# Kernel tuning notes

Hardware: AMD Instinct MI355X
Metric: run time of the kernel (lower is better)

The kernel has to match this reference:

```python
import jax, jax.numpy as jnp
import numpy as np

# --- dims (match init_kwargs) ---
B = 2048          # batch
BACK = 512        # backcast_length (in_dim of first layer)
UNITS = 512       # hidden units
FORE = 128        # forecast_length
TH = FORE         # thetas_dim (nb_harmonics=None)
NL = 4            # num_block_layers
NUM = 5           # grid intervals
K = 3             # spline order
MINP = 1          # min_period
NCOEF = NUM + K   # 8 spline coefficients per edge


def _grid(in_dim):
    # extended uniform grid over [-1,1] with K extra knots each side -> NUM+2K+1 points
    h = 2.0 / NUM
    pts = (np.arange(-K, NUM + K + 1) * h - 1.0).astype(np.float32)
    return jnp.asarray(np.tile(pts[None, :], (in_dim, 1)))


def _bspline(x, grid):
    # x: (B, in_dim), grid: (in_dim, NUM+2K+1) -> (B, in_dim, NUM+K)
    xe = x[:, :, None]
    g = grid[None]
    v = ((xe >= g[:, :, :-1]) & (xe < g[:, :, 1:])).astype(x.dtype)
    for p in range(1, K + 1):  # Cox-de Boor recursion, K is small & static
        v = (xe - g[:, :, :-(p + 1)]) / (g[:, :, p:-1] - g[:, :, :-(p + 1)]) * v[:, :, :-1] \
          + (g[:, :, p + 1:] - xe) / (g[:, :, p + 1:] - g[:, :, 1:-p]) * v[:, :, 1:]
    return v


def _kan(x, grid, coef, sb, ssp):
    # y[b,o] = sum_i sb[i,o]*silu(x[b,i]) + sum_i ssp[i,o]*sum_k B[b,i,k]*coef[i,o,k]
    # (mask == ones; scale_sp folded into coef to avoid (B,in,out) intermediate)
    bsp = _bspline(x, grid)                          # (B, in, NCOEF)
    base = jax.nn.silu(x)                            # (B, in)
    return base @ sb + jnp.einsum('bik,iok->bo', bsp, coef * ssp[:, :, None])


def _seasonal_basis():
    T = BACK + FORE
    lin = np.linspace(0.0, (T - 1) / T, T)           # linspace(centered=False)
    bl, fl = lin[:BACK], lin[BACK:]
    p1 = p2 = TH // 2                                # TH even
    f1 = np.linspace(0.0, T / MINP, p1)
    f2 = np.linspace(0.0, T / MINP, p2)
    Sb = np.concatenate([np.cos(2 * np.pi * f1[:, None] * bl),
                         np.sin(2 * np.pi * f2[:, None] * bl)]).astype(np.float32)
    Sf = np.concatenate([np.cos(2 * np.pi * f1[:, None] * fl),
                         np.sin(2 * np.pi * f2[:, None] * fl)]).astype(np.float32)
    return jnp.asarray(Sb), jnp.asarray(Sf)          # (TH, BACK), (TH, FORE)


def setup_inputs() -> dict:
    key = jax.random.key(0)
    ks = jax.random.split(key, 8)
    x = jax.random.uniform(ks[0], (B, BACK), jnp.float32, -1.0, 1.0)
    # fc KAN layers: first maps BACK->UNITS, rest UNITS->UNITS; BACK==UNITS so stack
    coef_fc = 0.1 * jax.random.normal(ks[1], (NL, UNITS, UNITS, NCOEF), jnp.float32)
    sb_fc = 0.3 * jax.random.normal(ks[2], (NL, UNITS, UNITS), jnp.float32)
    ssp_fc = 1.0 + 0.1 * jax.random.normal(ks[3], (NL, UNITS, UNITS), jnp.float32)
    # shared theta layer UNITS -> TH
    coef_th = 0.1 * jax.random.normal(ks[4], (UNITS, TH, NCOEF), jnp.float32)
    sb_th = 0.3 * jax.random.normal(ks[5], (UNITS, TH), jnp.float32)
    ssp_th = 1.0 + 0.1 * jax.random.normal(ks[6], (UNITS, TH), jnp.float32)
    return dict(x=x, coef_fc=coef_fc, sb_fc=sb_fc, ssp_fc=ssp_fc,
                coef_th=coef_th, sb_th=sb_th, ssp_th=ssp_th)


def reference(x, coef_fc, sb_fc, ssp_fc, coef_th, sb_th, ssp_th):
    grid = _grid(UNITS)  # BACK == UNITS, one grid serves all layers
    h = x
    for l in range(NL):  # static small layer loop (dropout p=0 / eval)
        h = _kan(h, grid, coef_fc[l], sb_fc[l], ssp_fc[l])
    theta = _kan(h, grid, coef_th, sb_th, ssp_th)  # theta_b_fc is theta_f_fc (shared)
    Sb, Sf = _seasonal_basis()
    backcast = theta @ Sb    # (B, BACK)
    forecast = theta @ Sf    # (B, FORE)
    return backcast, forecast
```

## Files before the change

### kernel.cpp

```cpp
#include <hip/hip_runtime.h>
#include <stdint.h>


typedef unsigned short u16;
typedef __attribute__((ext_vector_type(8))) short short8;
typedef __attribute__((ext_vector_type(4))) float f32x4;

#define NB 2048
#define KD 4608
#define NTH 128
#define NTT 640

__device__ __forceinline__ u16 f2bf(float f) {
  union { float f; uint32_t u; } c; c.f = f;
  return (u16)((c.u + 0x7FFFu + ((c.u >> 16) & 1u)) >> 16);
}

__device__ __forceinline__ void load_lds16(const void* g, void* lds) {
  __builtin_amdgcn_global_load_lds((const __attribute__((address_space(1))) void*)g,
                                   (__attribute__((address_space(3))) void*)lds, 16, 0, 0);
}

__device__ __forceinline__ void bspline8(float x, float* v8) {
  float g[12];
  #pragma unroll
  for (int j = 0; j < 12; ++j) g[j] = (float)((j - 3) * 0.4 - 1.0);
  float w[11];
  #pragma unroll
  for (int j = 0; j < 11; ++j) w[j] = (x >= g[j] && x < g[j+1]) ? 1.0f : 0.0f;
  #pragma unroll
  for (int p = 1; p <= 3; ++p) {
    #pragma unroll
    for (int j = 0; j < 11 - p; ++j) {
      const float i1 = 1.0f / (g[j+p] - g[j]);
      const float i2 = 1.0f / (g[j+p+1] - g[j+1]);
      w[j] = (x - g[j]) * i1 * w[j] + (g[j+p+1] - x) * i2 * w[j+1];
    }
  }
  #pragma unroll
  for (int j = 0; j < 8; ++j) v8[j] = w[j];
}

__device__ __forceinline__ void expand_one(float xv, u16* __restrict__ row, int i) {
  const float base = xv / (1.0f + __expf(-xv));
  float v[8];
  bspline8(xv, v);
  row[i] = f2bf(base);
  #pragma unroll
  for (int k = 0; k < 8; ++k) row[(1 + k) * 512 + i] = f2bf(v[k]);
}

__global__ __launch_bounds__(256)
void setup_kernel(const float* __restrict__ coef_fc, const float* __restrict__ sb_fc,
                  const float* __restrict__ ssp_fc,  const float* __restrict__ coef_th,
                  const float* __restrict__ sb_th,   const float* __restrict__ ssp_th,
                  u16* __restrict__ WtFc, u16* __restrict__ WtTh, float* __restrict__ S) {
  const int blk = blockIdx.x, tid = threadIdx.x;
  __shared__ u16 T[9 * 64 * 66];
  if (blk < 272) {
    const float *coef, *sb, *ssp; u16* Wt; int O, l, i0, o0;
    if (blk < 256) {
      coef = coef_fc; sb = sb_fc; ssp = ssp_fc; Wt = WtFc; O = 512;
      l = blk >> 6; i0 = ((blk >> 3) & 7) * 64; o0 = (blk & 7) * 64;
    } else {
      coef = coef_th; sb = sb_th; ssp = ssp_th; Wt = WtTh; O = 128;
      const int t = blk - 256;
      l = 0; i0 = (t >> 1) * 64; o0 = (t & 1) * 64;
    }
    #pragma unroll 4
    for (int pass = 0; pass < 16; ++pass) {
      const int o_loc = tid & 63;
      const int i_loc = pass * 4 + (tid >> 6);
      const size_t io = ((size_t)l * 512 + i0 + i_loc) * (size_t)O + o0 + o_loc;
      const float sspv = ssp[io];
      const float4 a = *(const float4*)(coef + io * 8);
      const float4 b = *(const float4*)(coef + io * 8 + 4);
      u16* t0 = T + i_loc * 66 + o_loc;
      t0[0 * 64 * 66] = f2bf(sb[io]);
      t0[1 * 64 * 66] = f2bf(a.x * sspv);
      t0[2 * 64 * 66] = f2bf(a.y * sspv);
      t0[3 * 64 * 66] = f2bf(a.z * sspv);
      t0[4 * 64 * 66] = f2bf(a.w * sspv);
      t0[5 * 64 * 66] = f2bf(b.x * sspv);
      t0[6 * 64 * 66] = f2bf(b.y * sspv);
      t0[7 * 64 * 66] = f2bf(b.z * sspv);
      t0[8 * 64 * 66] = f2bf(b.w * sspv);
    }
    __syncthreads();
    #pragma unroll
    for (int f = 0; f < 9; ++f)
      #pragma unroll 4
      for (int pass = 0; pass < 16; ++pass) {
        const int i_loc = tid & 63;
        const int o_loc = pass * 4 + (tid >> 6);
        Wt[((size_t)l * O + o0 + o_loc) * KD + f * 512 + i0 + i_loc] =
            T[(f * 64 + i_loc) * 66 + o_loc];
      }
  } else {
    const int base = (blk - 272) * 4096;
    #pragma unroll 4
    for (int q = 0; q < 16; ++q) {
      const int id = base + q * 256 + tid;
      const int j = id & 127, t = id >> 7;
      const int m = ((j & 63) * t) % 63;
      const float ang = (float)(6.283185307179586 * (double)m / 63.0);
      S[(size_t)j * NTT + t] = (j < 64) ? cosf(ang) : sinf(ang);
    }
  }
}

template<int NSUM>
__global__ __launch_bounds__(256)
void expand_kernel(const float* __restrict__ src, u16* __restrict__ Act) {
  #pragma unroll
  for (int q = 0; q < 4; ++q) {
    const int id = blockIdx.x * 1024 + q * 256 + threadIdx.x;
    const int b = id >> 9, i = id & 511;
    float xv;
    if (NSUM == 0) {
      xv = src[id];
    } else {
      float s = 0.f;
      #pragma unroll
      for (int t = 0; t < NSUM; ++t) s += src[(size_t)t * NB * 512 + id];
      xv = s;
    }
    expand_one(xv, Act + (size_t)b * KD, i);
  }
}

template<int N, int KITER>
__device__ __forceinline__ void gemm_body(const u16* __restrict__ A, const u16* __restrict__ Bt,
                                          float* __restrict__ Cp, int bx, int by, int bz,
                                          u16* sm) {
  u16* As0 = sm;          u16* Bs0 = sm + 8192;
  u16* As1 = sm + 16384;  u16* Bs1 = sm + 24576;
  const int tid  = threadIdx.x;
  const int wave = tid >> 6, lane = tid & 63;
  const int rowBase = bx * 128, colBase = by * 128;
  const int kb0 = bz * KITER;
  const int wr = wave >> 1, wc = wave & 1;
  const int lr = lane & 15, lk8 = lane >> 4;
  const int sRow   = lane >> 3;
  const int sChunk = (lane & 7) ^ sRow;

  f32x4 acc[4][4] = {};
  u16 *Asc = As0, *Bsc = Bs0, *Asn = As1, *Bsn = Bs1;

  #pragma unroll
  for (int j = 0; j < 4; ++j) {
    const int slot = (wave * 4 + j) * 8;
    load_lds16(A  + (size_t)(rowBase + slot + sRow) * KD + kb0 * 64 + sChunk * 8, Asc + slot * 64);
    load_lds16(Bt + (size_t)(colBase + slot + sRow) * KD + kb0 * 64 + sChunk * 8, Bsc + slot * 64);
  }
  asm volatile("s_waitcnt vmcnt(0)" ::: "memory");
  __builtin_amdgcn_s_barrier();

  for (int t = 0; t < KITER; ++t) {
    if (t + 1 < KITER) {
      const int kOff = (kb0 + t + 1) * 64;
      #pragma unroll
      for (int j = 0; j < 4; ++j) {
        const int slot = (wave * 4 + j) * 8;
        load_lds16(A  + (size_t)(rowBase + slot + sRow) * KD + kOff + sChunk * 8, Asn + slot * 64);
        load_lds16(Bt + (size_t)(colBase + slot + sRow) * KD + kOff + sChunk * 8, Bsn + slot * 64);
      }
    }
    #pragma unroll
    for (int ks = 0; ks < 2; ++ks) {
      short8 af[4], bf[4];
      const int kc = ks * 4 + lk8;
      #pragma unroll
      for (int m = 0; m < 4; ++m) {
        const int r = wr * 64 + m * 16 + lr;
        af[m] = *(const short8*)(Asc + r * 64 + ((kc ^ (r & 7)) * 8));
      }
      #pragma unroll
      for (int n = 0; n < 4; ++n) {
        const int r = wc * 64 + n * 16 + lr;
        bf[n] = *(const short8*)(Bsc + r * 64 + ((kc ^ (r & 7)) * 8));
      }
      #pragma unroll
      for (int m = 0; m < 4; ++m)
        #pragma unroll
        for (int n = 0; n < 4; ++n)
          acc[m][n] = __builtin_amdgcn_mfma_f32_16x16x32_bf16(af[m], bf[n], acc[m][n], 0, 0, 0);
    }
    asm volatile("s_waitcnt vmcnt(0)" ::: "memory");
    __builtin_amdgcn_s_barrier();
    u16* tp;
    tp = Asc; Asc = Asn; Asn = tp;
    tp = Bsc; Bsc = Bsn; Bsn = tp;
  }

  float* out = Cp + (size_t)bz * (size_t)NB * N;
  #pragma unroll
  for (int m = 0; m < 4; ++m) {
    const int row0 = rowBase + wr * 64 + m * 16 + (lane >> 4) * 4;
    #pragma unroll
    for (int n = 0; n < 4; ++n) {
      const int col = colBase + wc * 64 + n * 16 + lr;
      #pragma unroll
      for (int r = 0; r < 4; ++r)
        out[(size_t)(row0 + r) * N + col] = acc[m][n][r];
    }
  }
}

__global__ __launch_bounds__(256, 2)
void gemm_fc(const u16* __restrict__ A, const u16* __restrict__ Bt, float* __restrict__ Cp) {
  __shared__ __align__(16) u16 sm[4 * 8192];
  const int id  = blockIdx.x;
  const int xcd = id & 7;
  const int bz  = xcd >> 1;
  const int u   = id >> 3;
  const int bx  = ((u & 7) << 1) | (xcd & 1);
  const int by  = u >> 3;
  gemm_body<512, 18>(A, Bt, Cp, bx, by, bz, sm);
}

__global__ __launch_bounds__(256, 2)
void gemm_th(const u16* __restrict__ A, const u16* __restrict__ Bt, float* __restrict__ Cp) {
  __shared__ __align__(16) u16 sm[4 * 8192];
  gemm_body<NTH, 9>(A, Bt, Cp, blockIdx.x, 0, blockIdx.z, sm);
}

__global__ __launch_bounds__(256)
void proj_kernel(const float* __restrict__ Part, const float* __restrict__ S,
                 float* __restrict__ out) {
  __shared__ float Ts[64][129];
  const int tid = threadIdx.x;
  const int brow = blockIdx.x * 64, bcol = blockIdx.y * 64;
  for (int idx = tid; idx < 64 * 128; idx += 256) {
    const int r = idx >> 7, c = idx & 127;
    float s = 0.f;
    #pragma unroll
    for (int t = 0; t < 8; ++t)
      s += Part[(size_t)t * NB * NTH + (size_t)(brow + r) * NTH + c];
    Ts[r][c] = s;
  }
  __syncthreads();
  const int tx = tid & 15, ty = tid >> 4;
  const int r0 = ty * 4, c0 = tx * 4;
  float acc[4][4] = {};
  for (int k = 0; k < 128; ++k) {
    const float4 sv = *(const float4*)(S + (size_t)k * NTT + bcol + c0);
    #pragma unroll
    for (int rr = 0; rr < 4; ++rr) {
      const float tv = Ts[r0 + rr][k];
      acc[rr][0] += tv * sv.x; acc[rr][1] += tv * sv.y;
      acc[rr][2] += tv * sv.z; acc[rr][3] += tv * sv.w;
    }
  }
  #pragma unroll
  for (int rr = 0; rr < 4; ++rr) {
    const int b = brow + r0 + rr;
    #pragma unroll
    for (int cc = 0; cc < 4; ++cc) {
      const int t = bcol + c0 + cc;
      if (t < 512) out[(size_t)b * 512 + t] = acc[rr][cc];
      else         out[(size_t)NB * 512 + (size_t)b * NTH + (t - 512)] = acc[rr][cc];
    }
  }
}

extern "C" void kernel_launch(void* const* d_in, const int* in_sizes, int n_in,
                              void* d_out, int out_size, void* d_ws, size_t ws_size,
                              hipStream_t stream) {
  (void)in_sizes; (void)n_in; (void)out_size; (void)ws_size;
  const float* x       = (const float*)d_in[0];
  const float* coef_fc = (const float*)d_in[1];
  const float* sb_fc   = (const float*)d_in[2];
  const float* ssp_fc  = (const float*)d_in[3];
  const float* coef_th = (const float*)d_in[4];
  const float* sb_th   = (const float*)d_in[5];
  const float* ssp_th  = (const float*)d_in[6];
  float* out = (float*)d_out;

  u16*  WtFc = (u16*)d_ws;
  u16*  WtTh = WtFc + (size_t)4 * 512 * KD;
  u16*  Act  = WtTh + (size_t)NTH * KD;
  float* Part = (float*)(Act + (size_t)NB * KD);
  float* S    = Part + (size_t)4 * NB * 512;

  setup_kernel<<<dim3(292), dim3(256), 0, stream>>>(coef_fc, sb_fc, ssp_fc,
                                                    coef_th, sb_th, ssp_th,
                                                    WtFc, WtTh, S);
  expand_kernel<0><<<dim3(1024), dim3(256), 0, stream>>>(x, Act);
  for (int l = 0; l < 4; ++l) {
    gemm_fc<<<dim3(256), dim3(256), 0, stream>>>(Act, WtFc + (size_t)l * 512 * KD, Part);
    expand_kernel<4><<<dim3(1024), dim3(256), 0, stream>>>(Part, Act);
  }
  gemm_th<<<dim3(16, 1, 8), dim3(256), 0, stream>>>(Act, WtTh, Part);
  proj_kernel<<<dim3(32, 10), dim3(256), 0, stream>>>(Part, S, out);
}
```

Before: 241.5 us.

## Triple-buffer GEMM LDS pipeline, vectorize spline expansion, fuse first expand into setup

```diff
diff --git a/kernel.cpp b/kernel.cpp
--- a/kernel.cpp
+++ b/kernel.cpp
@@ -41,20 +41,32 @@
   for (int j = 0; j < 8; ++j) v8[j] = w[j];
 }
 
-__device__ __forceinline__ void expand_one(float xv, u16* __restrict__ row, int i) {
-  const float base = xv / (1.0f + __expf(-xv));
-  float v[8];
-  bspline8(xv, v);
-  row[i] = f2bf(base);
-  #pragma unroll
-  for (int k = 0; k < 8; ++k) row[(1 + k) * 512 + i] = f2bf(v[k]);
+__device__ __forceinline__ void expand_quad(const float* xv, u16* __restrict__ row, int i0) {
+  float base[4], v[4][8];
+  #pragma unroll
+  for (int e = 0; e < 4; ++e) {
+    base[e] = xv[e] / (1.0f + __expf(-xv[e]));
+    bspline8(xv[e], v[e]);
+  }
+  short4 s;
+  s.x = (short)f2bf(base[0]); s.y = (short)f2bf(base[1]);
+  s.z = (short)f2bf(base[2]); s.w = (short)f2bf(base[3]);
+  *(short4*)(row + i0) = s;
+  #pragma unroll
+  for (int f = 0; f < 8; ++f) {
+    s.x = (short)f2bf(v[0][f]); s.y = (short)f2bf(v[1][f]);
+    s.z = (short)f2bf(v[2][f]); s.w = (short)f2bf(v[3][f]);
+    *(short4*)(row + (1 + f) * 512 + i0) = s;
+  }
 }
 
 __global__ __launch_bounds__(256)
 void setup_kernel(const float* __restrict__ coef_fc, const float* __restrict__ sb_fc,
                   const float* __restrict__ ssp_fc,  const float* __restrict__ coef_th,
                   const float* __restrict__ sb_th,   const float* __restrict__ ssp_th,
-                  u16* __restrict__ WtFc, u16* __restrict__ WtTh, float* __restrict__ S) {
+                  const float* __restrict__ x,
+                  u16* __restrict__ WtFc, u16* __restrict__ WtTh,
+                  float* __restrict__ S,  u16* __restrict__ Act) {
   const int blk = blockIdx.x, tid = threadIdx.x;
   __shared__ u16 T[9 * 64 * 66];
   if (blk < 272) {
@@ -96,7 +108,7 @@
         Wt[((size_t)l * O + o0 + o_loc) * KD + f * 512 + i0 + i_loc] =
             T[(f * 64 + i_loc) * 66 + o_loc];
       }
-  } else {
+  } else if (blk < 292) {
     const int base = (blk - 272) * 4096;
     #pragma unroll 4
     for (int q = 0; q < 16; ++q) {
@@ -106,26 +118,67 @@
       const float ang = (float)(6.283185307179586 * (double)m / 63.0);
       S[(size_t)j * NTT + t] = (j < 64) ? cosf(ang) : sinf(ang);
     }
+  } else {
+    #pragma unroll
+    for (int q = 0; q < 4; ++q) {
+      const int qid = (blk - 292) * 1024 + q * 256 + tid;
+      const int b = qid >> 7, i0 = (qid & 127) * 4;
+      const float4 v = *(const float4*)(x + (size_t)qid * 4);
+      float xv[4] = {v.x, v.y, v.z, v.w};
+      expand_quad(xv, Act + (size_t)b * KD, i0);
+    }
   }
 }
 
 template<int NSUM>
 __global__ __launch_bounds__(256)
 void expand_kernel(const float* __restrict__ src, u16* __restrict__ Act) {
-  #pragma unroll
-  for (int q = 0; q < 4; ++q) {
-    const int id = blockIdx.x * 1024 + q * 256 + threadIdx.x;
-    const int b = id >> 9, i = id & 511;
-    float xv;
-    if (NSUM == 0) {
-      xv = src[id];
-    } else {
-      float s = 0.f;
+  const int qid = blockIdx.x * 256 + threadIdx.x;
+  const int b = qid >> 7, i0 = (qid & 127) * 4;
+  float xv[4] = {0.f, 0.f, 0.f, 0.f};
+  #pragma unroll
+  for (int t = 0; t < NSUM; ++t) {
+    const float4 v = *(const float4*)(src + (size_t)t * NB * 512 + (size_t)qid * 4);
+    xv[0] += v.x; xv[1] += v.y; xv[2] += v.z; xv[3] += v.w;
+  }
+  expand_quad(xv, Act + (size_t)b * KD, i0);
+}
+
+__device__ __forceinline__ void stage_tile(const u16* __restrict__ A, const u16* __restrict__ Bt,
+                                           u16* As, u16* Bs, int rowBase, int colBase,
+                                           int kOff, int wave, int lane) {
+  const int sRow   = lane >> 3;
+  const int sChunk = (lane & 7) ^ sRow;
+  #pragma unroll
+  for (int j = 0; j < 4; ++j) {
+    const int slot = (wave * 4 + j) * 8;
+    load_lds16(A  + (size_t)(rowBase + slot + sRow) * KD + kOff + sChunk * 8, As + slot * 64);
+    load_lds16(Bt + (size_t)(colBase + slot + sRow) * KD + kOff + sChunk * 8, Bs + slot * 64);
+  }
+}
+
+__device__ __forceinline__ void mma_step(const u16* As, const u16* Bs, f32x4 acc[4][4],
+                                         int wr, int wc, int lane) {
+  const int lr = lane & 15, lk8 = lane >> 4;
+  #pragma unroll
+  for (int ks = 0; ks < 2; ++ks) {
+    short8 af[4], bf[4];
+    const int kc = ks * 4 + lk8;
+    #pragma unroll
+    for (int m = 0; m < 4; ++m) {
+      const int r = wr * 64 + m * 16 + lr;
+      af[m] = *(const short8*)(As + r * 64 + ((kc ^ (r & 7)) * 8));
+    }
+    #pragma unroll
+    for (int n = 0; n < 4; ++n) {
+      const int r = wc * 64 + n * 16 + lr;
+      bf[n] = *(const short8*)(Bs + r * 64 + ((kc ^ (r & 7)) * 8));
+    }
+    #pragma unroll
+    for (int m = 0; m < 4; ++m)
       #pragma unroll
-      for (int t = 0; t < NSUM; ++t) s += src[(size_t)t * NB * 512 + id];
-      xv = s;
-    }
-    expand_one(xv, Act + (size_t)b * KD, i);
+      for (int n = 0; n < 4; ++n)
+        acc[m][n] = __builtin_amdgcn_mfma_f32_16x16x32_bf16(af[m], bf[n], acc[m][n], 0, 0, 0);
   }
 }
 
@@ -133,65 +186,35 @@
 __device__ __forceinline__ void gemm_body(const u16* __restrict__ A, const u16* __restrict__ Bt,
                                           float* __restrict__ Cp, int bx, int by, int bz,
                                           u16* sm) {
-  u16* As0 = sm;          u16* Bs0 = sm + 8192;
-  u16* As1 = sm + 16384;  u16* Bs1 = sm + 24576;
   const int tid  = threadIdx.x;
   const int wave = tid >> 6, lane = tid & 63;
   const int rowBase = bx * 128, colBase = by * 128;
   const int kb0 = bz * KITER;
   const int wr = wave >> 1, wc = wave & 1;
-  const int lr = lane & 15, lk8 = lane >> 4;
-  const int sRow   = lane >> 3;
-  const int sChunk = (lane & 7) ^ sRow;
+
+  u16 *Ac = sm,             *Bc = sm + 8192;
+  u16 *An = sm + 2 * 8192,  *Bn = sm + 3 * 8192;
+  u16 *Af = sm + 4 * 8192,  *Bf = sm + 5 * 8192;
 
   f32x4 acc[4][4] = {};
-  u16 *Asc = As0, *Bsc = Bs0, *Asn = As1, *Bsn = Bs1;
-
-  #pragma unroll
-  for (int j = 0; j < 4; ++j) {
-    const int slot = (wave * 4 + j) * 8;
-    load_lds16(A  + (size_t)(rowBase + slot + sRow) * KD + kb0 * 64 + sChunk * 8, Asc + slot * 64);
-    load_lds16(Bt + (size_t)(colBase + slot + sRow) * KD + kb0 * 64 + sChunk * 8, Bsc + slot * 64);
+
+  stage_tile(A, Bt, Ac, Bc, rowBase, colBase, (kb0 + 0) * 64, wave, lane);
+  stage_tile(A, Bt, An, Bn, rowBase, colBase, (kb0 + 1) * 64, wave, lane);
+
+  for (int t = 0; t < KITER - 1; ++t) {
+    asm volatile("s_waitcnt vmcnt(8)" ::: "memory");
+    __builtin_amdgcn_s_barrier();
+    if (t + 2 < KITER)
+      stage_tile(A, Bt, Af, Bf, rowBase, colBase, (kb0 + t + 2) * 64, wave, lane);
+    mma_step(Ac, Bc, acc, wr, wc, lane);
+    __builtin_amdgcn_s_barrier();
+    u16* tp;
+    tp = Ac; Ac = An; An = Af; Af = tp;
+    tp = Bc; Bc = Bn; Bn = Bf; Bf = tp;
   }
   asm volatile("s_waitcnt vmcnt(0)" ::: "memory");
   __builtin_amdgcn_s_barrier();
-
-  for (int t = 0; t < KITER; ++t) {
-    if (t + 1 < KITER) {
-      const int kOff = (kb0 + t + 1) * 64;
-      #pragma unroll
-      for (int j = 0; j < 4; ++j) {
-        const int slot = (wave * 4 + j) * 8;
-        load_lds16(A  + (size_t)(rowBase + slot + sRow) * KD + kOff + sChunk * 8, Asn + slot * 64);
-        load_lds16(Bt + (size_t)(colBase + slot + sRow) * KD + kOff + sChunk * 8, Bsn + slot * 64);
-      }
-    }
-    #pragma unroll
-    for (int ks = 0; ks < 2; ++ks) {
-      short8 af[4], bf[4];
-      const int kc = ks * 4 + lk8;
-      #pragma unroll
-      for (int m = 0; m < 4; ++m) {
-        const int r = wr * 64 + m * 16 + lr;
-        af[m] = *(const short8*)(Asc + r * 64 + ((kc ^ (r & 7)) * 8));
-      }
-      #pragma unroll
-      for (int n = 0; n < 4; ++n) {
-        const int r = wc * 64 + n * 16 + lr;
-        bf[n] = *(const short8*)(Bsc + r * 64 + ((kc ^ (r & 7)) * 8));
-      }
-      #pragma unroll
-      for (int m = 0; m < 4; ++m)
-        #pragma unroll
-        for (int n = 0; n < 4; ++n)
-          acc[m][n] = __builtin_amdgcn_mfma_f32_16x16x32_bf16(af[m], bf[n], acc[m][n], 0, 0, 0);
-    }
-    asm volatile("s_waitcnt vmcnt(0)" ::: "memory");
-    __builtin_amdgcn_s_barrier();
-    u16* tp;
-    tp = Asc; Asc = Asn; Asn = tp;
-    tp = Bsc; Bsc = Bsn; Bsn = tp;
-  }
+  mma_step(Ac, Bc, acc, wr, wc, lane);
 
   float* out = Cp + (size_t)bz * (size_t)NB * N;
   #pragma unroll
@@ -199,7 +222,7 @@
     const int row0 = rowBase + wr * 64 + m * 16 + (lane >> 4) * 4;
     #pragma unroll
     for (int n = 0; n < 4; ++n) {
-      const int col = colBase + wc * 64 + n * 16 + lr;
+      const int col = colBase + wc * 64 + n * 16 + (lane & 15);
       #pragma unroll
       for (int r = 0; r < 4; ++r)
         out[(size_t)(row0 + r) * N + col] = acc[m][n][r];
@@ -207,9 +230,9 @@
   }
 }
 
-__global__ __launch_bounds__(256, 2)
+__global__ __launch_bounds__(256, 1)
 void gemm_fc(const u16* __restrict__ A, const u16* __restrict__ Bt, float* __restrict__ Cp) {
-  __shared__ __align__(16) u16 sm[4 * 8192];
+  __shared__ __align__(16) u16 sm[6 * 8192];
   const int id  = blockIdx.x;
   const int xcd = id & 7;
   const int bz  = xcd >> 1;
@@ -219,9 +242,9 @@
   gemm_body<512, 18>(A, Bt, Cp, bx, by, bz, sm);
 }
 
-__global__ __launch_bounds__(256, 2)
+__global__ __launch_bounds__(256, 1)
 void gemm_th(const u16* __restrict__ A, const u16* __restrict__ Bt, float* __restrict__ Cp) {
-  __shared__ __align__(16) u16 sm[4 * 8192];
+  __shared__ __align__(16) u16 sm[6 * 8192];
   gemm_body<NTH, 9>(A, Bt, Cp, blockIdx.x, 0, blockIdx.z, sm);
 }
 
@@ -283,10 +306,9 @@
   float* Part = (float*)(Act + (size_t)NB * KD);
   float* S    = Part + (size_t)4 * NB * 512;
 
-  setup_kernel<<<dim3(292), dim3(256), 0, stream>>>(coef_fc, sb_fc, ssp_fc,
-                                                    coef_th, sb_th, ssp_th,
-                                                    WtFc, WtTh, S);
-  expand_kernel<0><<<dim3(1024), dim3(256), 0, stream>>>(x, Act);
+  setup_kernel<<<dim3(548), dim3(256), 0, stream>>>(coef_fc, sb_fc, ssp_fc,
+                                                    coef_th, sb_th, ssp_th, x,
+                                                    WtFc, WtTh, S, Act);
   for (int l = 0; l < 4; ++l) {
     gemm_fc<<<dim3(256), dim3(256), 0, stream>>>(Act, WtFc + (size_t)l * 512 * KD, Part);
     expand_kernel<4><<<dim3(1024), dim3(256), 0, stream>>>(Part, Act);
```

After: 240.1 us. No clear change (-0.6%).
